# Kernel tuning notes

Hardware: AMD Instinct MI355X
Metric: run time of the kernel (lower is better)

Reference implementation:

```python
import jax, jax.numpy as jnp
import numpy as np

V = 12000; WE = 1000; FEAT = 2048; FE = 1024; H = 1024; AH = 512; NREG = 36; B = 128; T = 17
PAD_ID = 0


def _lstm_cell(x, h, c, wih, whh, bih, bhh):
    # torch LSTMCell: gates ordered (input, forget, cell, output)
    g = x @ wih.T + h @ whh.T + bih + bhh
    i, f, gg, o = jnp.split(g, 4, axis=-1)
    c_new = jax.nn.sigmoid(f) * c + jax.nn.sigmoid(i) * jnp.tanh(gg)
    h_new = jax.nn.sigmoid(o) * jnp.tanh(c_new)
    return h_new, c_new


def setup_inputs() -> dict:
    key = jax.random.key(0)
    ks = jax.random.split(key, 24)
    s = 0.02
    emb_w = jax.random.normal(ks[0], (V, WE), jnp.float32) * s
    emb_w = emb_w.at[PAD_ID].set(0.0)  # padding_idx row is zero
    inp = {
        'fc_feats': jax.random.normal(ks[1], (B, FEAT), jnp.float32),
        'att_feats': jax.random.normal(ks[2], (B, NREG, FEAT), jnp.float32),
        'captions': jax.random.randint(ks[3], (B, T), 0, V, jnp.int64),
        'emb_w': emb_w,
        'fc_w': jax.random.normal(ks[4], (FEAT, FE), jnp.float32) * s,
        'fc_b': jnp.zeros((FE,), jnp.float32),
        'atte_w': jax.random.normal(ks[5], (FEAT, FE), jnp.float32) * s,
        'atte_b': jnp.zeros((FE,), jnp.float32),
        'ctx_w': jax.random.normal(ks[6], (FE, AH), jnp.float32) * s,
        'ctx_b': jnp.zeros((AH,), jnp.float32),
        'attl_wih': jax.random.normal(ks[7], (4 * H, H + FE + WE), jnp.float32) * s,
        'attl_whh': jax.random.normal(ks[8], (4 * H, H), jnp.float32) * s,
        'attl_bih': jnp.zeros((4 * H,), jnp.float32),
        'attl_bhh': jnp.zeros((4 * H,), jnp.float32),
        'h2att_w': jax.random.normal(ks[9], (H, AH), jnp.float32) * s,
        'h2att_b': jnp.zeros((AH,), jnp.float32),
        'alpha_w': jax.random.normal(ks[10], (AH,), jnp.float32) * s,
        'alpha_b': jnp.zeros((), jnp.float32),
        'langl_wih': jax.random.normal(ks[11], (4 * H, FE + H), jnp.float32) * s,
        'langl_whh': jax.random.normal(ks[12], (4 * H, H), jnp.float32) * s,
        'langl_bih': jnp.zeros((4 * H,), jnp.float32),
        'langl_bhh': jnp.zeros((4 * H,), jnp.float32),
        'cls_w': jax.random.normal(ks[13], (H, V), jnp.float32) * s,
        'cls_b': jnp.zeros((V,), jnp.float32),
    }
    return inp


def _forward(fc_feats, att_feats, captions, emb_w, fc_w, fc_b, atte_w, atte_b,
             ctx_w, ctx_b, attl_wih, attl_whh, attl_bih, attl_bhh,
             h2att_w, h2att_b, alpha_w, alpha_b,
             langl_wih, langl_whh, langl_bih, langl_bhh, cls_w, cls_b):
    # _prepare_features (eval mode: dropout is identity)
    fc_e = jax.nn.relu(fc_feats @ fc_w + fc_b)                 # [B, FE]
    att_e = jax.nn.relu(att_feats @ atte_w + atte_b)           # [B, N, FE]
    p_att = att_e @ ctx_w + ctx_b                              # [B, N, AH]
    bsz = fc_feats.shape[0]
    h0 = jnp.zeros((bsz, H), fc_feats.dtype)

    def step(carry, it):
        h_att, c_att, h_lang, c_lang = carry
        w = jax.nn.relu(emb_w[it])                             # [B, WE]
        x_att = jnp.concatenate([h_lang, fc_e, w], axis=1)
        h_att, c_att = _lstm_cell(x_att, h_att, c_att, attl_wih, attl_whh, attl_bih, attl_bhh)
        # Attention
        hq = h_att @ h2att_w + h2att_b                          # [B, AH]
        e = jnp.tanh(p_att + hq[:, None, :]) @ alpha_w + alpha_b  # [B, N]
        alpha = jax.nn.softmax(e, axis=1)
        att_res = jnp.einsum('bn,bnd->bd', alpha, att_e)        # [B, FE]
        x_lang = jnp.concatenate([att_res, h_att], axis=1)
        h_lang, c_lang = _lstm_cell(x_lang, h_lang, c_lang, langl_wih, langl_whh, langl_bih, langl_bhh)
        logprobs = jax.nn.log_softmax(h_lang @ cls_w + cls_b, axis=1)  # [B, V]
        return (h_att, c_att, h_lang, c_lang), logprobs

    its = captions[:, :-1].T  # [T-1, B]
    _, outs = jax.lax.scan(step, (h0, h0, h0, h0), its)
    return jnp.transpose(outs, (1, 0, 2))  # [B, T-1, V]


def reference(fc_feats, att_feats, captions, emb_w, fc_w, fc_b, atte_w, atte_b,
              ctx_w, ctx_b, attl_wih, attl_whh, attl_bih, attl_bhh,
              h2att_w, h2att_b, alpha_w, alpha_b,
              langl_wih, langl_whh, langl_bih, langl_bhh, cls_w, cls_b):
    return _forward(fc_feats, att_feats, captions, emb_w, fc_w, fc_b, atte_w, atte_b,
                    ctx_w, ctx_b, attl_wih, attl_whh, attl_bih, attl_bhh,
                    h2att_w, h2att_b, alpha_w, alpha_b,
                    langl_wih, langl_whh, langl_bih, langl_bhh, cls_w, cls_b)
```

## Files before the change

kernel.cpp:

```cpp
#include <hip/hip_runtime.h>
#include <cstddef>
#include <cstdint>

constexpr int CV    = 12000;
constexpr int CVP2  = 12288;
constexpr int CWE   = 1000;
constexpr int CFEAT = 2048;
constexpr int CFE   = 1024;
constexpr int CH    = 1024;
constexpr int CAH   = 512;
constexpr int CNREG = 36;
constexpr int CB    = 128;
constexpr int CT    = 17;
constexpr int G4    = 4096;
constexpr int XH    = 2048;
constexpr int XL3   = 3072;

#define CDIV(a,b) (((a)+(b)-1)/(b))

typedef __bf16 bf16_t;
typedef __bf16 bf16x8 __attribute__((ext_vector_type(8)));
typedef __bf16 bf16x4 __attribute__((ext_vector_type(4)));
typedef float  f32x4  __attribute__((ext_vector_type(4)));

typedef __attribute__((address_space(3))) uint32_t lds_u32;
typedef const __attribute__((address_space(1))) uint32_t glb_u32;

struct Seg { const bf16_t* A; const bf16_t* W; int lda, ldw, kt; };

template<bool RELU, bool OUTBF, int SWZ>
__global__ __launch_bounds__(256)
void pre_gemm(Seg s0, int inner, const float* __restrict__ bias1,
              void* __restrict__ Cout, int ldc)
{
    const int tid = threadIdx.x;
    const int wid = tid >> 6, lane = tid & 63;
    const int wr = wid >> 1, wc = wid & 1;
    const int llo = lane & 15, lhi = lane >> 4;
    const int nb = gridDim.x, id = blockIdx.x;
    const int sw = (id & 7) * (nb >> 3) + (id >> 3);
    int m0, n0;
    if (SWZ == 1)      { n0 = (sw / inner) * 64;  m0 = (sw % inner) * 128; }
    else if (SWZ == 2) { m0 = (sw / inner) * 128; n0 = (sw % inner) * 64;  }
    else {
        const int xcd = id & 7, idx = id >> 3;
        m0 = (((xcd >> 2) << 3) + (idx & 7)) * 128;
        n0 = (((xcd & 3) << 4) + (idx >> 3)) * 64;
    }

    __shared__ __align__(16) uint8_t sm[2][24576];

    const int TT = s0.kt;
    f32x4 acc[4][2] = {};
    uint4 ra[4], rb[2];
    const int srow = tid >> 3, sc = tid & 7;
    const int cswz = (sc ^ (srow & 7)) << 4;

    auto load_tile = [&](int ti) {
        const int k0 = ti << 6;
        #pragma unroll
        for (int i = 0; i < 4; ++i)
            ra[i] = *(const uint4*)(s0.A + (size_t)(m0 + i * 32 + srow) * s0.lda + k0 + sc * 8);
        #pragma unroll
        for (int i = 0; i < 2; ++i)
            rb[i] = *(const uint4*)(s0.W + (size_t)(n0 + i * 32 + srow) * s0.ldw + k0 + sc * 8);
    };
    auto write_tile = [&](int buf) {
        uint8_t* base = sm[buf];
        #pragma unroll
        for (int i = 0; i < 4; ++i) *(uint4*)(base + (i * 32 + srow) * 128 + cswz) = ra[i];
        #pragma unroll
        for (int i = 0; i < 2; ++i) *(uint4*)(base + 16384 + (i * 32 + srow) * 128 + cswz) = rb[i];
    };
    auto compute = [&](int buf) {
        const uint8_t* base = sm[buf];
        const int r7 = llo & 7;
        #pragma unroll
        for (int kk = 0; kk < 2; ++kk) {
            const int coff = ((kk * 4 + lhi) ^ r7) << 4;
            bf16x8 af[4], bg[2];
            #pragma unroll
            for (int fm = 0; fm < 4; ++fm)
                af[fm] = *(const bf16x8*)(base + (wr * 64 + fm * 16 + llo) * 128 + coff);
            #pragma unroll
            for (int fn = 0; fn < 2; ++fn)
                bg[fn] = *(const bf16x8*)(base + 16384 + (wc * 32 + fn * 16 + llo) * 128 + coff);
            #pragma unroll
            for (int fm = 0; fm < 4; ++fm)
                #pragma unroll
                for (int fn = 0; fn < 2; ++fn)
                    acc[fm][fn] = __builtin_amdgcn_mfma_f32_16x16x32_bf16(
                        af[fm], bg[fn], acc[fm][fn], 0, 0, 0);
        }
    };

    load_tile(0); write_tile(0);
    load_tile(1);
    __syncthreads();
    int cur = 0;
    for (int ti = 0; ti < TT; ++ti) {
        if (ti + 1 < TT) write_tile(cur ^ 1);
        if (ti + 2 < TT) load_tile(ti + 2);
        compute(cur);
        __syncthreads();
        cur ^= 1;
    }

    if (OUTBF) {
        bf16_t* st = (bf16_t*)sm[0];
        #pragma unroll
        for (int fn = 0; fn < 2; ++fn) {
            const int lcol = wc * 32 + fn * 16 + llo;
            const float b = bias1 ? bias1[n0 + lcol] : 0.f;
            #pragma unroll
            for (int fm = 0; fm < 4; ++fm)
                #pragma unroll
                for (int r = 0; r < 4; ++r) {
                    float v = acc[fm][fn][r] + b;
                    if (RELU) v = fmaxf(v, 0.f);
                    st[(wr * 64 + fm * 16 + lhi * 4 + r) * 64 + lcol] = (bf16_t)v;
                }
        }
        __syncthreads();
        #pragma unroll
        for (int i = 0; i < 4; ++i) {
            const int q = tid + i * 256;
            const int row = q >> 3, ch = q & 7;
            *(uint4*)((bf16_t*)Cout + (size_t)(m0 + row) * ldc + n0 + ch * 8)
                = *(const uint4*)&st[row * 64 + ch * 8];
        }
    } else {
        const int colb = n0 + wc * 32;
        const int rowb = m0 + wr * 64 + lhi * 4;
        #pragma unroll
        for (int fn = 0; fn < 2; ++fn) {
            const int col = colb + fn * 16 + llo;
            const float b = bias1 ? bias1[col] : 0.f;
            #pragma unroll
            for (int fm = 0; fm < 4; ++fm)
                #pragma unroll
                for (int r = 0; r < 4; ++r) {
                    float v = acc[fm][fn][r] + b;
                    if (RELU) v = fmaxf(v, 0.f);
                    ((float*)Cout)[(size_t)(rowb + fm * 16 + r) * ldc + col] = v;
                }
        }
    }
}

__global__ __launch_bounds__(256)
void cls_gemm(const bf16_t* __restrict__ A, const bf16_t* __restrict__ W,
              const float* __restrict__ bias, bf16_t* __restrict__ Cout)
{
    const int tid = threadIdx.x;
    const int wid = tid >> 6, lane = tid & 63;
    const int wr = wid >> 1, wc = wid & 1;
    const int llo = lane & 15, lhi = lane >> 4;
    const int id = blockIdx.x;
    const int xcd = id & 7, idx = id >> 3;
    const int mg = xcd & 1, ng = xcd >> 1;
    const int m0 = (mg * 8 + (idx & 7)) * 128;
    const int n0 = (ng * 24 + (idx >> 3)) * 128;

    __shared__ __align__(16) uint8_t smA[2][8192];
    __shared__ __align__(16) uint8_t smB[2][8192];

    constexpr int TT = 32;
    f32x4 acc[4][4] = {};

    const int scq = (lane & 3) ^ ((lane >> 3) & 3);
    auto stage = [&](int buf, int ti) {
        const int k0 = ti << 5;
        #pragma unroll
        for (int i = 0; i < 2; ++i) {
            const int cq = wid * 64 + lane + i * 256;
            const int row = cq >> 2;
            const bf16_t* ga = A + (size_t)(m0 + row) * CH + k0 + scq * 8;
            __builtin_amdgcn_global_load_lds((glb_u32*)ga,
                (lds_u32*)(smA[buf] + (wid * 64 + i * 256) * 16 + lane * 16), 16, 0, 0);
            const bf16_t* gb = W + (size_t)(n0 + row) * CH + k0 + scq * 8;
            __builtin_amdgcn_global_load_lds((glb_u32*)gb,
                (lds_u32*)(smB[buf] + (wid * 64 + i * 256) * 16 + lane * 16), 16, 0, 0);
        }
    };
    auto compute = [&](int buf) {
        bf16x8 af[4], bg[4];
        #pragma unroll
        for (int fm = 0; fm < 4; ++fm) {
            const int r = wr * 64 + fm * 16 + llo;
            const int p = lhi ^ ((r >> 1) & 3);
            af[fm] = *(const bf16x8*)(smA[buf] + r * 64 + p * 16);
        }
        #pragma unroll
        for (int fn = 0; fn < 4; ++fn) {
            const int r = wc * 64 + fn * 16 + llo;
            const int p = lhi ^ ((r >> 1) & 3);
            bg[fn] = *(const bf16x8*)(smB[buf] + r * 64 + p * 16);
        }
        #pragma unroll
        for (int fm = 0; fm < 4; ++fm)
            #pragma unroll
            for (int fn = 0; fn < 4; ++fn)
                acc[fm][fn] = __builtin_amdgcn_mfma_f32_16x16x32_bf16(
                    af[fm], bg[fn], acc[fm][fn], 0, 0, 0);
    };

    stage(0, 0);
    __syncthreads();
    int cur = 0;
    for (int ti = 0; ti < TT; ++ti) {
        if (ti + 1 < TT) stage(cur ^ 1, ti + 1);
        compute(cur);
        __syncthreads();
        cur ^= 1;
    }

    bf16_t* st = (bf16_t*)smA;
    #pragma unroll
    for (int fn = 0; fn < 4; ++fn) {
        const int lcol = wc * 64 + fn * 16 + llo;
        const int col = n0 + lcol;
        const float b = (col < CV) ? bias[col] : 0.f;
        #pragma unroll
        for (int fm = 0; fm < 4; ++fm)
            #pragma unroll
            for (int r = 0; r < 4; ++r)
                st[(wr * 64 + fm * 16 + lhi * 4 + r) * 128 + lcol]
                    = (bf16_t)(acc[fm][fn][r] + b);
    }
    __syncthreads();
    #pragma unroll
    for (int i = 0; i < 8; ++i) {
        const int q = tid + i * 256;
        const int row = q >> 4, ch = q & 15;
        *(uint4*)(Cout + (size_t)(m0 + row) * CVP2 + n0 + ch * 8)
            = *(const uint4*)&st[row * 128 + ch * 8];
    }
}

template<int TAG>
__global__ __launch_bounds__(256)
void gate_split(const bf16_t* __restrict__ A, int lda,
                const bf16_t* __restrict__ W, int ldw, int ktz,
                bf16_t* __restrict__ gpart)
{
    const int tid = threadIdx.x;
    const int w = tid >> 6, lane = tid & 63;
    const int llo = lane & 15, lhi = lane >> 4;
    const int n0 = blockIdx.x * 16;
    const int z  = blockIdx.y;
    const int kb = z * ktz;

    __shared__ __align__(16) uint8_t smA[2][16384];
    __shared__ __align__(16) uint8_t smB[2][2048];

    f32x4 acc0 = {0.f,0.f,0.f,0.f}, acc1 = {0.f,0.f,0.f,0.f};

    const int arow = tid >> 3, ac = tid & 7;
    const int asc = ac ^ (arow & 7);
    const int wvoff = (tid >> 6) * 1024;

    auto stage = [&](int buf, int ti) {
        const int k0 = (kb + ti) << 6;
        #pragma unroll
        for (int i = 0; i < 4; ++i) {
            const bf16_t* gp = A + (size_t)(arow + i * 32) * lda + k0 + asc * 8;
            __builtin_amdgcn_global_load_lds((glb_u32*)gp,
                (lds_u32*)(smA[buf] + i * 4096 + wvoff), 16, 0, 0);
        }
        if (tid < 128) {
            const int brow = tid >> 3, bc = tid & 7;
            const int bsc = bc ^ (brow & 7);
            const bf16_t* gp = W + (size_t)(n0 + brow) * ldw + k0 + bsc * 8;
            __builtin_amdgcn_global_load_lds((glb_u32*)gp,
                (lds_u32*)(smB[buf] + wvoff), 16, 0, 0);
        }
    };
    auto compute = [&](int buf) {
        const int r7 = llo & 7;
        #pragma unroll
        for (int kk = 0; kk < 2; ++kk) {
            const int coff = ((kk * 4 + lhi) ^ r7) << 4;
            bf16x8 a0 = *(const bf16x8*)(smA[buf] + (w * 32 + llo) * 128 + coff);
            bf16x8 a1 = *(const bf16x8*)(smA[buf] + (w * 32 + 16 + llo) * 128 + coff);
            bf16x8 bb = *(const bf16x8*)(smB[buf] + llo * 128 + coff);
            acc0 = __builtin_amdgcn_mfma_f32_16x16x32_bf16(a0, bb, acc0, 0, 0, 0);
            acc1 = __builtin_amdgcn_mfma_f32_16x16x32_bf16(a1, bb, acc1, 0, 0, 0);
        }
    };

    stage(0, 0);
    __syncthreads();
    int cur = 0;
    for (int ti = 0; ti < ktz; ++ti) {
        if (ti + 1 < ktz) stage(cur ^ 1, ti + 1);
        compute(cur);
        __syncthreads();
        cur ^= 1;
    }

    bf16_t* gp = gpart + (size_t)z * CB * G4;
    const int col = n0 + llo;
    #pragma unroll
    for (int r = 0; r < 4; ++r) {
        gp[(size_t)(w * 32 + lhi * 4 + r) * G4 + col] = (bf16_t)acc0[r];
        gp[(size_t)(w * 32 + 16 + lhi * 4 + r) * G4 + col] = (bf16_t)acc1[r];
    }
}

__global__ __launch_bounds__(1024)
void lstm_attn(const bf16_t* __restrict__ gpart, const bf16_t* __restrict__ gpre_fc,
               const bf16_t* __restrict__ gemb,
               const float* __restrict__ cbias, float* __restrict__ c_att,
               const bf16_t* __restrict__ p_att, const bf16_t* __restrict__ att_e,
               const bf16_t* __restrict__ h2att_wT, const float* __restrict__ h2att_b,
               const float* __restrict__ alpha_w, const float* __restrict__ alpha_b,
               bf16_t* __restrict__ xh_nxt, bf16_t* __restrict__ xl_cur)
{
    __shared__ float sh[CH];
    __shared__ float shq[CAH];
    __shared__ float se[64], salpha[64];
    const int b = blockIdx.x, tid = threadIdx.x;

    {
        const int j = tid;
        float g0 = 0.f, g1 = 0.f, g2 = 0.f, g3 = 0.f;
        #pragma unroll
        for (int z = 0; z < 4; ++z) {
            bf16x4 g = *(const bf16x4*)(gpart + (size_t)z * CB * G4 + (size_t)b * G4 + 4 * j);
            g0 += (float)g[0]; g1 += (float)g[1]; g2 += (float)g[2]; g3 += (float)g[3];
        }
        f32x4 cb = *(const f32x4*)(cbias + 4 * j);
        bf16x4 gf4 = *(const bf16x4*)(gpre_fc + (size_t)b * G4 + 4 * j);
        bf16x4 ge4 = *(const bf16x4*)(gemb + (size_t)b * G4 + 4 * j);
        const float gi = g0 + cb[0] + (float)gf4[0] + (float)ge4[0];
        const float gf = g1 + cb[1] + (float)gf4[1] + (float)ge4[1];
        const float gg = g2 + cb[2] + (float)gf4[2] + (float)ge4[2];
        const float go = g3 + cb[3] + (float)gf4[3] + (float)ge4[3];
        const float si = 1.f / (1.f + expf(-gi));
        const float sf = 1.f / (1.f + expf(-gf));
        const float so = 1.f / (1.f + expf(-go));
        const float cn = sf * c_att[b * CH + j] + si * tanhf(gg);
        const float hn = so * tanhf(cn);
        c_att[b * CH + j] = cn;
        sh[j] = hn;
        const bf16_t hb = (bf16_t)hn;
        xh_nxt[(size_t)b * XH + 1024 + j] = hb;
        xl_cur[(size_t)b * XL3 + 1024 + j] = hb;
    }
    __syncthreads();

    {
        const int q2 = tid & 1, n = tid >> 1;
        const bf16_t* wrow = h2att_wT + (size_t)n * CH + q2 * 512;
        float s = 0.f;
        #pragma unroll 4
        for (int k = 0; k < 512; k += 8) {
            bf16x8 w8 = *(const bf16x8*)(wrow + k);
            #pragma unroll
            for (int j = 0; j < 8; ++j) s = fmaf((float)w8[j], sh[q2 * 512 + k + j], s);
        }
        s += __shfl_xor(s, 1);
        if (q2 == 0) shq[n] = s + h2att_b[n];
    }
    __syncthreads();

    {
        const int wave = tid >> 6, lane = tid & 63;
        for (int n = wave; n < CNREG; n += 16) {
            const bf16_t* pr = p_att + ((size_t)b * CNREG + n) * CAH;
            float s = 0.f;
            #pragma unroll
            for (int q = 0; q < CAH / 64; ++q) {
                const int d = lane + q * 64;
                s += alpha_w[d] * tanhf((float)pr[d] + shq[d]);
            }
            for (int off = 32; off; off >>= 1) s += __shfl_down(s, off);
            if (lane == 0) se[n] = s + alpha_b[0];
        }
    }
    __syncthreads();

    {
        float mx = -1e30f;
        for (int n = 0; n < CNREG; ++n) mx = fmaxf(mx, se[n]);
        float sum = 0.f;
        for (int n = 0; n < CNREG; ++n) sum += expf(se[n] - mx);
        if (tid < CNREG) salpha[tid] = expf(se[tid] - mx) / sum;
    }
    __syncthreads();

    {
        const int d = tid;
        float s = 0.f;
        const bf16_t* ae = att_e + (size_t)b * CNREG * CFE + d;
        #pragma unroll 4
        for (int n = 0; n < CNREG; ++n)
            s = fmaf(salpha[n], (float)ae[(size_t)n * CFE], s);
        xl_cur[(size_t)b * XL3 + d] = (bf16_t)s;
    }
}

__global__ __launch_bounds__(256)
void lstm_flat(const bf16_t* __restrict__ gpart, const float* __restrict__ cbias,
               float* __restrict__ c,
               bf16_t* __restrict__ xh_nxt, bf16_t* __restrict__ xl_nxt,
               bf16_t* __restrict__ h_all, int t)
{
    const int idx = blockIdx.x * 256 + threadIdx.x;
    const int b = idx >> 10, j = idx & 1023;
    float g0 = 0.f, g1 = 0.f, g2 = 0.f, g3 = 0.f;
    #pragma unroll
    for (int z = 0; z < 4; ++z) {
        bf16x4 g = *(const bf16x4*)(gpart + (size_t)z * CB * G4 + (size_t)b * G4 + 4 * j);
        g0 += (float)g[0]; g1 += (float)g[1]; g2 += (float)g[2]; g3 += (float)g[3];
    }
    f32x4 cb = *(const f32x4*)(cbias + 4 * j);
    const float si = 1.f / (1.f + expf(-(g0 + cb[0])));
    const float sf = 1.f / (1.f + expf(-(g1 + cb[1])));
    const float so = 1.f / (1.f + expf(-(g3 + cb[3])));
    const float cn = sf * c[idx] + si * tanhf(g2 + cb[2]);
    const float hn = so * tanhf(cn);
    c[idx] = cn;
    const bf16_t hb = (bf16_t)hn;
    xh_nxt[(size_t)b * XH + j] = hb;
    xl_nxt[(size_t)b * XL3 + 2048 + j] = hb;
    h_all[((size_t)b * (CT - 1) + t) * CH + j] = hb;
}

__global__ void convert_pad(const float* __restrict__ src, bf16_t* __restrict__ dst,
                            int C, int Cp)
{
    const int r = blockIdx.y;
    const int c = blockIdx.x * 256 + threadIdx.x;
    if (c >= Cp) return;
    dst[(size_t)r * Cp + c] = (c < C) ? (bf16_t)src[(size_t)r * C + c] : (bf16_t)0.f;
}

__global__ void convert_perm(const float* __restrict__ src, int srcld, int scol0,
                             int valid, bf16_t* __restrict__ dst, int dstld, int dcol0,
                             int ncols)
{
    const int rp = blockIdx.y;
    const int c = blockIdx.x * 256 + threadIdx.x;
    if (c >= ncols) return;
    const int rs = (rp & 3) * 1024 + (rp >> 2);
    const float v = (c < valid) ? src[(size_t)rs * srcld + scol0 + c] : 0.f;
    dst[(size_t)rp * dstld + dcol0 + c] = (bf16_t)v;
}

__global__ void bias_perm(const float* __restrict__ bih, const float* __restrict__ bhh,
                          float* __restrict__ dst)
{
    const int rp = blockIdx.x * 256 + threadIdx.x;
    if (rp >= G4) return;
    const int rs = (rp & 3) * 1024 + (rp >> 2);
    dst[rp] = bih[rs] + bhh[rs];
}

__global__ __launch_bounds__(256)
void transpose_convert(const float* __restrict__ src, bf16_t* __restrict__ dst,
                       int K, int N)
{
    __shared__ float tile[32][33];
    const int n0 = blockIdx.x * 32, k0 = blockIdx.y * 32;
    const int tx = threadIdx.x & 31, ty = threadIdx.x >> 5;
    #pragma unroll
    for (int i = 0; i < 4; ++i) {
        const int k = k0 + ty + i * 8, n = n0 + tx;
        tile[ty + i * 8][tx] = (k < K && n < N) ? src[(size_t)k * N + n] : 0.f;
    }
    __syncthreads();
    #pragma unroll
    for (int i = 0; i < 4; ++i) {
        const int n = n0 + ty + i * 8, k = k0 + tx;
        if (n < N && k < K) dst[(size_t)n * K + k] = (bf16_t)tile[tx][ty + i * 8];
    }
}

__global__ void emb_all(const float* __restrict__ emb_w,
                        const int* __restrict__ captions, bf16_t* __restrict__ w_emb)
{
    const int r = blockIdx.y;
    const int j = blockIdx.x * 256 + threadIdx.x;
    const int t = r >> 7, b = r & 127;
    const int tok = captions[b * CT + t];
    const float v = (j < CWE) ? fmaxf(emb_w[(size_t)tok * CWE + j], 0.f) : 0.f;
    w_emb[(size_t)r * 1024 + j] = (bf16_t)v;
}

__global__ __launch_bounds__(256)
void logsoftmax_bf(const bf16_t* __restrict__ lg, float* __restrict__ out)
{
    __shared__ float red[4];
    const int r = blockIdx.x, tid = threadIdx.x;
    const bf16_t* row = lg + (size_t)r * CVP2;

    float v[48];
    float mx = -1e30f;
    #pragma unroll
    for (int i = 0; i < 6; ++i) {
        const int c = tid + i * 256;
        if (c < 1500) {
            bf16x8 x = *(const bf16x8*)(row + c * 8);
            #pragma unroll
            for (int j = 0; j < 8; ++j) {
                v[i * 8 + j] = (float)x[j];
                mx = fmaxf(mx, v[i * 8 + j]);
            }
        } else {
            #pragma unroll
            for (int j = 0; j < 8; ++j) v[i * 8 + j] = -1e30f;
        }
    }
    for (int off = 32; off; off >>= 1) mx = fmaxf(mx, __shfl_down(mx, off));
    if ((tid & 63) == 0) red[tid >> 6] = mx;
    __syncthreads();
    mx = fmaxf(fmaxf(red[0], red[1]), fmaxf(red[2], red[3]));
    __syncthreads();

    float sum = 0.f;
    #pragma unroll
    for (int i = 0; i < 6; ++i)
        if (tid + i * 256 < 1500)
            #pragma unroll
            for (int j = 0; j < 8; ++j) sum += expf(v[i * 8 + j] - mx);
    for (int off = 32; off; off >>= 1) sum += __shfl_down(sum, off);
    if ((tid & 63) == 0) red[tid >> 6] = sum;
    __syncthreads();
    sum = red[0] + red[1] + red[2] + red[3];
    const float lse = mx + logf(sum);

    #pragma unroll
    for (int i = 0; i < 6; ++i) {
        const int c = tid + i * 256;
        if (c < 1500) {
            float* o = out + (size_t)r * CV + c * 8;
            float4 a = make_float4(v[i*8+0]-lse, v[i*8+1]-lse, v[i*8+2]-lse, v[i*8+3]-lse);
            float4 bq = make_float4(v[i*8+4]-lse, v[i*8+5]-lse, v[i*8+6]-lse, v[i*8+7]-lse);
            *(float4*)o = a;
            *(float4*)(o + 4) = bq;
        }
    }
}

extern "C" void kernel_launch(void* const* d_in, const int* in_sizes, int n_in,
                              void* d_out, int out_size, void* d_ws, size_t ws_size,
                              hipStream_t stream)
{
    const float* fc_feats  = (const float*)d_in[0];
    const float* att_feats = (const float*)d_in[1];
    const int*   captions  = (const int*)  d_in[2];
    const float* emb_w     = (const float*)d_in[3];
    const float* fc_w      = (const float*)d_in[4];
    const float* fc_b      = (const float*)d_in[5];
    const float* atte_w    = (const float*)d_in[6];
    const float* atte_b    = (const float*)d_in[7];
    const float* ctx_w     = (const float*)d_in[8];
    const float* ctx_b     = (const float*)d_in[9];
    const float* attl_wih  = (const float*)d_in[10];
    const float* attl_whh  = (const float*)d_in[11];
    const float* attl_bih  = (const float*)d_in[12];
    const float* attl_bhh  = (const float*)d_in[13];
    const float* h2att_w   = (const float*)d_in[14];
    const float* h2att_b   = (const float*)d_in[15];
    const float* alpha_w   = (const float*)d_in[16];
    const float* alpha_b   = (const float*)d_in[17];
    const float* langl_wih = (const float*)d_in[18];
    const float* langl_whh = (const float*)d_in[19];
    const float* langl_bih = (const float*)d_in[20];
    const float* langl_bhh = (const float*)d_in[21];
    const float* cls_w     = (const float*)d_in[22];
    const float* cls_b     = (const float*)d_in[23];

    float* out = (float*)d_out;

    char* p = (char*)d_ws;
    auto alloc_bf = [&](size_t e) { bf16_t* q = (bf16_t*)p; p += e * 2; return q; };
    auto alloc_f  = [&](size_t e) { float*  q = (float*) p; p += e * 4; return q; };

    bf16_t* Wcat_att    = alloc_bf((size_t)G4 * XH);
    bf16_t* Wcat_lang   = alloc_bf((size_t)G4 * XL3);
    bf16_t* Win_fc      = alloc_bf((size_t)G4 * 1024);
    bf16_t* Win_emb     = alloc_bf((size_t)G4 * 1024);
    bf16_t* fc_wT_b     = alloc_bf((size_t)CFE * CFEAT);
    bf16_t* atte_wT_b   = alloc_bf((size_t)CFE * CFEAT);
    bf16_t* ctx_wT_b    = alloc_bf((size_t)CAH * CFE);
    bf16_t* h2att_wT_b  = alloc_bf((size_t)CAH * CH);
    bf16_t* cls_wT_b    = alloc_bf((size_t)CVP2 * CH);
    bf16_t* fc_feats_b  = alloc_bf((size_t)CB * CFEAT);
    bf16_t* att_feats_b = alloc_bf((size_t)CB * CNREG * CFEAT);
    bf16_t* att_e_b     = alloc_bf((size_t)CB * CNREG * CFE);
    bf16_t* w_emb       = alloc_bf((size_t)(CT - 1) * CB * 1024);
    bf16_t* fc_e_b      = alloc_bf((size_t)CB * CFE);
    bf16_t* gpre_fc     = alloc_bf((size_t)CB * G4);
    bf16_t* xh0         = alloc_bf((size_t)CB * XH);
    bf16_t* xh1         = alloc_bf((size_t)CB * XH);
    bf16_t* xl3a        = alloc_bf((size_t)CB * XL3);
    bf16_t* xl3b        = alloc_bf((size_t)CB * XL3);
    bf16_t* h_all       = alloc_bf((size_t)CB * (CT - 1) * CH);
    bf16_t* p_att       = alloc_bf((size_t)CB * CNREG * CAH);
    bf16_t* gpart       = alloc_bf((size_t)4 * CB * G4);
    float*  cbias_att   = alloc_f (G4);
    float*  cbias_lang  = alloc_f (G4);
    float*  c_att       = alloc_f ((size_t)CB * CH);
    float*  c_lang      = alloc_f ((size_t)CB * CH);

    bf16_t* Gemb   = att_feats_b;
    bf16_t* logits = Wcat_att;

    hipMemsetAsync(xh0,    0, (size_t)CB * XH * 2, stream);
    hipMemsetAsync(xh1,    0, (size_t)CB * XH * 2, stream);
    hipMemsetAsync(xl3a,   0, (size_t)CB * XL3 * 2, stream);
    hipMemsetAsync(xl3b,   0, (size_t)CB * XL3 * 2, stream);
    hipMemsetAsync(c_att,  0, (size_t)CB * CH * 4, stream);
    hipMemsetAsync(c_lang, 0, (size_t)CB * CH * 4, stream);
    hipMemsetAsync(cls_wT_b + (size_t)CV * CH, 0, (size_t)(CVP2 - CV) * CH * 2, stream);

    const dim3 blk(256);
    auto mk = [](const bf16_t* A, int lda, const bf16_t* W, int ldw, int kt) {
        return Seg{A, W, lda, ldw, kt};
    };

    convert_perm<<<dim3(4, G4), blk, 0, stream>>>(attl_wih, 3048, 0, 1024, Wcat_att, XH, 0, 1024);
    convert_perm<<<dim3(4, G4), blk, 0, stream>>>(attl_whh, 1024, 0, 1024, Wcat_att, XH, 1024, 1024);
    convert_perm<<<dim3(4, G4), blk, 0, stream>>>(attl_wih, 3048, 1024, 1024, Win_fc, 1024, 0, 1024);
    convert_perm<<<dim3(4, G4), blk, 0, stream>>>(attl_wih, 3048, 2048, 1000, Win_emb, 1024, 0, 1024);
    convert_perm<<<dim3(8, G4), blk, 0, stream>>>(langl_wih, 2048, 0, 2048, Wcat_lang, XL3, 0, 2048);
    convert_perm<<<dim3(4, G4), blk, 0, stream>>>(langl_whh, 1024, 0, 1024, Wcat_lang, XL3, 2048, 1024);
    bias_perm<<<16, blk, 0, stream>>>(attl_bih, attl_bhh, cbias_att);
    bias_perm<<<16, blk, 0, stream>>>(langl_bih, langl_bhh, cbias_lang);
    convert_pad<<<dim3(8, CB), blk, 0, stream>>>(fc_feats, fc_feats_b, CFEAT, CFEAT);
    convert_pad<<<dim3(8, CB * CNREG), blk, 0, stream>>>(att_feats, att_feats_b, CFEAT, CFEAT);
    transpose_convert<<<dim3(CFE/32, CFEAT/32), blk, 0, stream>>>(fc_w,    fc_wT_b,    CFEAT, CFE);
    transpose_convert<<<dim3(CFE/32, CFEAT/32), blk, 0, stream>>>(atte_w,  atte_wT_b,  CFEAT, CFE);
    transpose_convert<<<dim3(CAH/32, CFE/32),   blk, 0, stream>>>(ctx_w,   ctx_wT_b,   CFE,   CAH);
    transpose_convert<<<dim3(CAH/32, CH/32),    blk, 0, stream>>>(h2att_w, h2att_wT_b, CH,    CAH);
    transpose_convert<<<dim3(CDIV(CV,32), CH/32), blk, 0, stream>>>(cls_w, cls_wT_b,   CH,    CV);
    emb_all<<<dim3(4, (CT - 1) * CB), blk, 0, stream>>>(emb_w, captions, w_emb);

    pre_gemm<true,true,2><<<16, blk, 0, stream>>>(
        mk(fc_feats_b, CFEAT, fc_wT_b, CFEAT, 32), 16, fc_b, fc_e_b, CFE);
    pre_gemm<true,true,2><<<576, blk, 0, stream>>>(
        mk(att_feats_b, CFEAT, atte_wT_b, CFEAT, 32), 16, atte_b, att_e_b, CFE);
    pre_gemm<false,true,2><<<288, blk, 0, stream>>>(
        mk(att_e_b, CFE, ctx_wT_b, CFE, 16), 8, ctx_b, p_att, CAH);
    pre_gemm<false,true,1><<<64, blk, 0, stream>>>(
        mk(fc_e_b, CFE, Win_fc, 1024, 16), 1, nullptr, gpre_fc, G4);
    pre_gemm<false,true,3><<<1024, blk, 0, stream>>>(
        mk(w_emb, 1024, Win_emb, 1024, 16), 0, nullptr, Gemb, G4);

    for (int t = 0; t < CT - 1; ++t) {
        bf16_t* xh_cur = (t & 1) ? xh1 : xh0;
        bf16_t* xh_nxt = (t & 1) ? xh0 : xh1;
        bf16_t* xl_cur = (t & 1) ? xl3b : xl3a;
        bf16_t* xl_nxt = (t & 1) ? xl3a : xl3b;

        gate_split<0><<<dim3(256, 4), blk, 0, stream>>>(
            xh_cur, XH, Wcat_att, XH, 8, gpart);

        lstm_attn<<<CB, dim3(1024), 0, stream>>>(
            gpart, gpre_fc, Gemb + (size_t)t * CB * G4, cbias_att, c_att,
            p_att, att_e_b, h2att_wT_b, h2att_b, alpha_w, alpha_b,
            xh_nxt, xl_cur);

        gate_split<1><<<dim3(256, 4), blk, 0, stream>>>(
            xl_cur, XL3, Wcat_lang, XL3, 12, gpart);

        lstm_flat<<<512, blk, 0, stream>>>(
            gpart, cbias_lang, c_lang, xh_nxt, xl_nxt, h_all, t);
    }

    cls_gemm<<<1536, blk, 0, stream>>>(h_all, cls_wT_b, cls_b, logits);
    logsoftmax_bf<<<2048, blk, 0, stream>>>(logits, out);
}
```

Before: 1.837 ms.

## Stage pre-GEMM tiles directly into LDS with global_load_lds and halve K tile

```diff
diff --git a/kernel.cpp b/kernel.cpp
--- a/kernel.cpp
+++ b/kernel.cpp
@@ -48,66 +48,64 @@
         n0 = (((xcd & 3) << 4) + (idx >> 3)) * 64;
     }
 
-    __shared__ __align__(16) uint8_t sm[2][24576];
+    __shared__ __align__(16) uint8_t smA[2][8192];
+    __shared__ __align__(16) uint8_t smB[2][4096];
 
     const int TT = s0.kt;
     f32x4 acc[4][2] = {};
-    uint4 ra[4], rb[2];
-    const int srow = tid >> 3, sc = tid & 7;
-    const int cswz = (sc ^ (srow & 7)) << 4;
-
-    auto load_tile = [&](int ti) {
-        const int k0 = ti << 6;
-        #pragma unroll
-        for (int i = 0; i < 4; ++i)
-            ra[i] = *(const uint4*)(s0.A + (size_t)(m0 + i * 32 + srow) * s0.lda + k0 + sc * 8);
-        #pragma unroll
-        for (int i = 0; i < 2; ++i)
-            rb[i] = *(const uint4*)(s0.W + (size_t)(n0 + i * 32 + srow) * s0.ldw + k0 + sc * 8);
-    };
-    auto write_tile = [&](int buf) {
-        uint8_t* base = sm[buf];
-        #pragma unroll
-        for (int i = 0; i < 4; ++i) *(uint4*)(base + (i * 32 + srow) * 128 + cswz) = ra[i];
-        #pragma unroll
-        for (int i = 0; i < 2; ++i) *(uint4*)(base + 16384 + (i * 32 + srow) * 128 + cswz) = rb[i];
+
+    const int scq = (lane & 3) ^ ((lane >> 3) & 3);
+    auto stage = [&](int buf, int ti) {
+        const int k0 = ti << 5;
+        #pragma unroll
+        for (int i = 0; i < 2; ++i) {
+            const int cq = wid * 64 + lane + i * 256;
+            const int row = cq >> 2;
+            const bf16_t* ga = s0.A + (size_t)(m0 + row) * s0.lda + k0 + scq * 8;
+            __builtin_amdgcn_global_load_lds((glb_u32*)ga,
+                (lds_u32*)(smA[buf] + (wid * 64 + i * 256) * 16 + lane * 16), 16, 0, 0);
+        }
+        {
+            const int row = tid >> 2;
+            const bf16_t* gb = s0.W + (size_t)(n0 + row) * s0.ldw + k0 + scq * 8;
+            __builtin_amdgcn_global_load_lds((glb_u32*)gb,
+                (lds_u32*)(smB[buf] + wid * 1024 + lane * 16), 16, 0, 0);
+        }
     };
     auto compute = [&](int buf) {
-        const uint8_t* base = sm[buf];
-        const int r7 = llo & 7;
-        #pragma unroll
-        for (int kk = 0; kk < 2; ++kk) {
-            const int coff = ((kk * 4 + lhi) ^ r7) << 4;
-            bf16x8 af[4], bg[2];
-            #pragma unroll
-            for (int fm = 0; fm < 4; ++fm)
-                af[fm] = *(const bf16x8*)(base + (wr * 64 + fm * 16 + llo) * 128 + coff);
+        bf16x8 af[4], bg[2];
+        #pragma unroll
+        for (int fm = 0; fm < 4; ++fm) {
+            const int r = wr * 64 + fm * 16 + llo;
+            const int p = lhi ^ ((r >> 1) & 3);
+            af[fm] = *(const bf16x8*)(smA[buf] + r * 64 + p * 16);
+        }
+        #pragma unroll
+        for (int fn = 0; fn < 2; ++fn) {
+            const int r = wc * 32 + fn * 16 + llo;
+            const int p = lhi ^ ((r >> 1) & 3);
+            bg[fn] = *(const bf16x8*)(smB[buf] + r * 64 + p * 16);
+        }
+        #pragma unroll
+        for (int fm = 0; fm < 4; ++fm)
             #pragma unroll
             for (int fn = 0; fn < 2; ++fn)
-                bg[fn] = *(const bf16x8*)(base + 16384 + (wc * 32 + fn * 16 + llo) * 128 + coff);
-            #pragma unroll
-            for (int fm = 0; fm < 4; ++fm)
-                #pragma unroll
-                for (int fn = 0; fn < 2; ++fn)
-                    acc[fm][fn] = __builtin_amdgcn_mfma_f32_16x16x32_bf16(
-                        af[fm], bg[fn], acc[fm][fn], 0, 0, 0);
-        }
+                acc[fm][fn] = __builtin_amdgcn_mfma_f32_16x16x32_bf16(
+                    af[fm], bg[fn], acc[fm][fn], 0, 0, 0);
     };
 
-    load_tile(0); write_tile(0);
-    load_tile(1);
+    stage(0, 0);
     __syncthreads();
     int cur = 0;
     for (int ti = 0; ti < TT; ++ti) {
-        if (ti + 1 < TT) write_tile(cur ^ 1);
-        if (ti + 2 < TT) load_tile(ti + 2);
+        if (ti + 1 < TT) stage(cur ^ 1, ti + 1);
         compute(cur);
         __syncthreads();
         cur ^= 1;
     }
 
     if (OUTBF) {
-        bf16_t* st = (bf16_t*)sm[0];
+        bf16_t* st = (bf16_t*)smA;
         #pragma unroll
         for (int fn = 0; fn < 2; ++fn) {
             const int lcol = wc * 32 + fn * 16 + llo;
@@ -640,15 +638,15 @@
     emb_all<<<dim3(4, (CT - 1) * CB), blk, 0, stream>>>(emb_w, captions, w_emb);
 
     pre_gemm<true,true,2><<<16, blk, 0, stream>>>(
-        mk(fc_feats_b, CFEAT, fc_wT_b, CFEAT, 32), 16, fc_b, fc_e_b, CFE);
+        mk(fc_feats_b, CFEAT, fc_wT_b, CFEAT, 64), 16, fc_b, fc_e_b, CFE);
     pre_gemm<true,true,2><<<576, blk, 0, stream>>>(
-        mk(att_feats_b, CFEAT, atte_wT_b, CFEAT, 32), 16, atte_b, att_e_b, CFE);
+        mk(att_feats_b, CFEAT, atte_wT_b, CFEAT, 64), 16, atte_b, att_e_b, CFE);
     pre_gemm<false,true,2><<<288, blk, 0, stream>>>(
-        mk(att_e_b, CFE, ctx_wT_b, CFE, 16), 8, ctx_b, p_att, CAH);
+        mk(att_e_b, CFE, ctx_wT_b, CFE, 32), 8, ctx_b, p_att, CAH);
     pre_gemm<false,true,1><<<64, blk, 0, stream>>>(
-        mk(fc_e_b, CFE, Win_fc, 1024, 16), 1, nullptr, gpre_fc, G4);
+        mk(fc_e_b, CFE, Win_fc, 1024, 32), 1, nullptr, gpre_fc, G4);
     pre_gemm<false,true,3><<<1024, blk, 0, stream>>>(
-        mk(w_emb, 1024, Win_emb, 1024, 16), 0, nullptr, Gemb, G4);
+        mk(w_emb, 1024, Win_emb, 1024, 32), 0, nullptr, Gemb, G4);
 
     for (int t = 0; t < CT - 1; ++t) {
         bf16_t* xh_cur = (t & 1) ? xh1 : xh0;
```

New measurement: 1.575 ms, median of 2. 14.3% less time.
